# Performance work log

Hardware: AMD Instinct MI355X
Metric: run time of the kernel (lower is better)

The kernel has to match this reference:

```python
import jax, jax.numpy as jnp
import numpy as np

STATE_DIM = 512
N_AGENTS = 16
N_ACTIONS = 32
EMBED = 512          # mixing_embed_dim
Q_IN = STATE_DIM + N_AGENTS * N_ACTIONS  # 1024 (coma_critic arch)
ROWS = 32768         # bs * ts = 64 * 512


def _linear_params(key, d_in, d_out):
    kw, kb = jax.random.split(key)
    bound = 1.0 / np.sqrt(d_in)
    W = jax.random.uniform(kw, (d_in, d_out), minval=-bound, maxval=bound, dtype=jnp.float32)
    b = jax.random.uniform(kb, (d_out,), minval=-bound, maxval=bound, dtype=jnp.float32)
    return W, b


def setup_inputs() -> dict:
    key = jax.random.key(0)
    ks = jax.random.split(key, 8)
    states = jax.random.normal(ks[0], (ROWS, STATE_DIM), dtype=jnp.float32)
    actions = jax.random.uniform(ks[1], (ROWS, N_AGENTS * N_ACTIONS), dtype=jnp.float32)
    Qw1, Qb1 = _linear_params(ks[2], Q_IN, EMBED)
    Qw2, Qb2 = _linear_params(ks[3], EMBED, EMBED)
    Qw3, Qb3 = _linear_params(ks[4], EMBED, 1)
    Vw1, Vb1 = _linear_params(ks[5], STATE_DIM, EMBED)
    Vw2, Vb2 = _linear_params(ks[6], EMBED, EMBED)
    Vw3, Vb3 = _linear_params(ks[7], EMBED, 1)
    return {
        "states": states, "actions": actions,
        "Qw1": Qw1, "Qb1": Qb1, "Qw2": Qw2, "Qb2": Qb2, "Qw3": Qw3, "Qb3": Qb3,
        "Vw1": Vw1, "Vb1": Vb1, "Vw2": Vw2, "Vb2": Vb2, "Vw3": Vw3, "Vb3": Vb3,
    }


def _mlp3(x, W1, b1, W2, b2, W3, b3):
    h = jax.nn.relu(x @ W1 + b1)
    h = jax.nn.relu(h @ W2 + b2)
    return h @ W3 + b3


def reference(states, actions,
              Qw1, Qb1, Qw2, Qb2, Qw3, Qb3,
              Vw1, Vb1, Vw2, Vb2, Vw3, Vb3):
    # coma_critic arch: inputs = cat([states, joint-action one-hots], dim=1)
    inputs = jnp.concatenate([states, actions], axis=1)  # [bs*ts, Q_IN]
    q_outputs = _mlp3(inputs, Qw1, Qb1, Qw2, Qb2, Qw3, Qb3)  # [bs*ts, 1]
    v_outputs = _mlp3(states, Vw1, Vb1, Vw2, Vb2, Vw3, Vb3)  # [bs*ts, 1]
    return q_outputs, v_outputs
```

## Files before the change

### kernel.cpp

```cpp
#include <hip/hip_runtime.h>


#define ROWS 32768
#define EMBED 512

using frag_ab = __attribute__((ext_vector_type(8))) short;
using f32x4   = __attribute__((ext_vector_type(4))) float;

__device__ __forceinline__ unsigned short f2bf(float f) {
    unsigned int u = __builtin_bit_cast(unsigned int, f);
    return (unsigned short)((u + 0x7fffu + ((u >> 16) & 1u)) >> 16);
}

__device__ __forceinline__ unsigned pk2rne(float lo, float hi) {
    return (unsigned)f2bf(lo) | ((unsigned)f2bf(hi) << 16);
}

__device__ __forceinline__ void async_copy16(const void* g, void* l) {
    __builtin_amdgcn_global_load_lds(
        (const __attribute__((address_space(1))) unsigned int*)g,
        (__attribute__((address_space(3))) unsigned int*)l, 16, 0, 0);
}

__device__ __forceinline__ void decode_mn(int L, int& mi, int& nq) {
    nq = (L >> 3) & 7;
    mi = ((L >> 6) << 3) | (L & 7);
}

__global__ __launch_bounds__(256)
void prep(const float* __restrict__ states, const float* __restrict__ actions,
          const float* __restrict__ Qw1, const float* __restrict__ Qw2,
          const float* __restrict__ Vw1, const float* __restrict__ Vw2,
          const float* __restrict__ qb3, const float* __restrict__ vb3,
          unsigned short* __restrict__ X,
          unsigned short* __restrict__ Qw1t, unsigned short* __restrict__ Qw2t,
          unsigned short* __restrict__ Vw1t, unsigned short* __restrict__ Vw2t,
          float* __restrict__ out) {
    const int b = blockIdx.x, tid = threadIdx.x;
    if (b < 4096) {
        int c = b * 256 + tid;
        int m = c >> 5, col = (c & 31) * 32;
        const float* src = (col < 512) ? states + (size_t)m * 512 + col
                                       : actions + (size_t)m * 512 + (col - 512);
        float4 f[8];
#pragma unroll
        for (int i = 0; i < 8; i++) f[i] = ((const float4*)src)[i];
        uint4* dst = (uint4*)(X + (size_t)m * 1024 + col);
#pragma unroll
        for (int i = 0; i < 4; i++)
            dst[i] = make_uint4(pk2rne(f[2*i].x,   f[2*i].y),
                                pk2rne(f[2*i].z,   f[2*i].w),
                                pk2rne(f[2*i+1].x, f[2*i+1].y),
                                pk2rne(f[2*i+1].z, f[2*i+1].w));
    } else if (b < 4736) {
        int g = (b - 4096) * 256 + tid;
        const float* W; unsigned short* O; int n, k0, ldo;
        if (g < 65536) {
            int o = g * 8; n = o >> 10; k0 = o & 1023; W = Qw1; O = Qw1t; ldo = 1024;
        } else {
            g -= 65536;
            int seg = g >> 15, r = g & 32767, o = r * 8;
            n = o >> 9; k0 = o & 511; ldo = 512;
            W = (seg == 0) ? Qw2 : (seg == 1) ? Vw1 : Vw2;
            O = (seg == 0) ? Qw2t : (seg == 1) ? Vw1t : Vw2t;
        }
        float v[8];
#pragma unroll
        for (int j = 0; j < 8; j++) v[j] = W[(size_t)(k0 + j) * 512 + n];
        *(uint4*)(O + (size_t)n * ldo + k0) =
            make_uint4(pk2rne(v[0], v[1]), pk2rne(v[2], v[3]),
                       pk2rne(v[4], v[5]), pk2rne(v[6], v[7]));
    } else {
        int i = (b - 4736) * 256 + tid;
        out[i] = (i < ROWS) ? qb3[0] : vb3[0];
    }
}

__global__ __launch_bounds__(256)
void layer1(const unsigned short* __restrict__ X,
            const unsigned short* __restrict__ Qw1t,
            const unsigned short* __restrict__ Vw1t,
            const float* __restrict__ Qb1, const float* __restrict__ Vb1,
            unsigned short* __restrict__ h1Q, unsigned short* __restrict__ h1V) {
    __shared__ __align__(16) unsigned short As[2 * 4096];
    __shared__ __align__(16) unsigned short Bs[2 * 4096];

    const int tid = threadIdx.x, wave = tid >> 6, lane = tid & 63;
    int mi, nq; decode_mn(blockIdx.x, mi, nq);
    const bool isV = nq >= 4;
    const int bn = (nq & 3) * 128;
    const int bm = mi * 128;
    const int K = isV ? 512 : 1024;
    const unsigned short* Wt = isV ? Vw1t : Qw1t;
    const float* bias = isV ? Vb1 : Qb1;
    unsigned short* H = isV ? h1V : h1Q;

    const int wm = (wave & 1) * 64, wn = (wave >> 1) * 64;
    const int lrow = lane & 15, quad = lane >> 4;
    f32x4 acc[4][4] = {};

    const int lin  = wave * 1024 + lane * 16;
    const int rowS = lin >> 6, colS = (lin & 63) >> 1;
    const unsigned short* gA0 = X  + (size_t)(bm + rowS)      * 1024 + colS;
    const unsigned short* gA1 = X  + (size_t)(bm + rowS + 64) * 1024 + colS;
    const unsigned short* gB0 = Wt + (size_t)(bn + rowS)      * K + colS;
    const unsigned short* gB1 = Wt + (size_t)(bn + rowS + 64) * K + colS;
    unsigned short* ldsA0 = As + wave * 512;
    unsigned short* ldsA1 = As + 2048 + wave * 512;
    unsigned short* ldsB0 = Bs + wave * 512;
    unsigned short* ldsB1 = Bs + 2048 + wave * 512;

    for (int k0 = 0; k0 < K; k0 += 64) {
        async_copy16(gA0,      ldsA0);
        async_copy16(gA0 + 32, ldsA0 + 4096);
        async_copy16(gA1,      ldsA1);
        async_copy16(gA1 + 32, ldsA1 + 4096);
        async_copy16(gB0,      ldsB0);
        async_copy16(gB0 + 32, ldsB0 + 4096);
        async_copy16(gB1,      ldsB1);
        async_copy16(gB1 + 32, ldsB1 + 4096);
        gA0 += 64; gA1 += 64; gB0 += 64; gB1 += 64;
        __syncthreads();

#pragma unroll
        for (int s = 0; s < 2; s++) {
            frag_ab af[4], bfr[4];
#pragma unroll
            for (int i = 0; i < 4; i++)
                af[i] = *(const frag_ab*)&As[s * 4096 + (wm + i * 16 + lrow) * 32 + quad * 8];
#pragma unroll
            for (int j = 0; j < 4; j++)
                bfr[j] = *(const frag_ab*)&Bs[s * 4096 + (wn + j * 16 + lrow) * 32 + quad * 8];
#pragma unroll
            for (int i = 0; i < 4; i++)
#pragma unroll
                for (int j = 0; j < 4; j++)
                    acc[i][j] = __builtin_amdgcn_mfma_f32_16x16x32_bf16(
                        af[i], bfr[j], acc[i][j], 0, 0, 0);
        }
        __syncthreads();
    }

#pragma unroll
    for (int j = 0; j < 4; j++) {
        const int col = bn + wn + j * 16 + lrow;
        const float bc = bias[col];
#pragma unroll
        for (int i = 0; i < 4; i++) {
            const int row0 = bm + wm + i * 16 + quad * 4;
#pragma unroll
            for (int r = 0; r < 4; r++) {
                float v = acc[i][j][r] + bc;
                v = v > 0.0f ? v : 0.0f;
                H[(size_t)(row0 + r) * EMBED + col] = f2bf(v);
            }
        }
    }
}

__global__ __launch_bounds__(256)
void layer2(const unsigned short* __restrict__ h1Q,
            const unsigned short* __restrict__ h1V,
            const unsigned short* __restrict__ Qw2t,
            const unsigned short* __restrict__ Vw2t,
            const float* __restrict__ Qb2, const float* __restrict__ Vb2,
            const float* __restrict__ Qw3, const float* __restrict__ Vw3,
            float* __restrict__ out) {
    __shared__ __align__(16) unsigned short As[2 * 4096];
    __shared__ __align__(16) unsigned short Bs[2 * 4096];

    const int tid = threadIdx.x, wave = tid >> 6, lane = tid & 63;
    int mi, nq; decode_mn(blockIdx.x, mi, nq);
    const bool isV = nq >= 4;
    const int bn = (nq & 3) * 128;
    const int bm = mi * 128;
    const unsigned short* A  = isV ? h1V : h1Q;
    const unsigned short* Wt = isV ? Vw2t : Qw2t;
    const float* bias = isV ? Vb2 : Qb2;
    const float* w3   = isV ? Vw3 : Qw3;
    float* op = out + (isV ? ROWS : 0);

    const int wm = (wave & 1) * 64, wn = (wave >> 1) * 64;
    const int lrow = lane & 15, quad = lane >> 4;
    f32x4 acc[4][4] = {};

    const int lin  = wave * 1024 + lane * 16;
    const int rowS = lin >> 6, colS = (lin & 63) >> 1;
    const unsigned short* gA0 = A  + (size_t)(bm + rowS)      * 512 + colS;
    const unsigned short* gA1 = A  + (size_t)(bm + rowS + 64) * 512 + colS;
    const unsigned short* gB0 = Wt + (size_t)(bn + rowS)      * 512 + colS;
    const unsigned short* gB1 = Wt + (size_t)(bn + rowS + 64) * 512 + colS;
    unsigned short* ldsA0 = As + wave * 512;
    unsigned short* ldsA1 = As + 2048 + wave * 512;
    unsigned short* ldsB0 = Bs + wave * 512;
    unsigned short* ldsB1 = Bs + 2048 + wave * 512;

    for (int k0 = 0; k0 < 512; k0 += 64) {
        async_copy16(gA0,      ldsA0);
        async_copy16(gA0 + 32, ldsA0 + 4096);
        async_copy16(gA1,      ldsA1);
        async_copy16(gA1 + 32, ldsA1 + 4096);
        async_copy16(gB0,      ldsB0);
        async_copy16(gB0 + 32, ldsB0 + 4096);
        async_copy16(gB1,      ldsB1);
        async_copy16(gB1 + 32, ldsB1 + 4096);
        gA0 += 64; gA1 += 64; gB0 += 64; gB1 += 64;
        __syncthreads();

#pragma unroll
        for (int s = 0; s < 2; s++) {
            frag_ab af[4], bfr[4];
#pragma unroll
            for (int i = 0; i < 4; i++)
                af[i] = *(const frag_ab*)&As[s * 4096 + (wm + i * 16 + lrow) * 32 + quad * 8];
#pragma unroll
            for (int j = 0; j < 4; j++)
                bfr[j] = *(const frag_ab*)&Bs[s * 4096 + (wn + j * 16 + lrow) * 32 + quad * 8];
#pragma unroll
            for (int i = 0; i < 4; i++)
#pragma unroll
                for (int j = 0; j < 4; j++)
                    acc[i][j] = __builtin_amdgcn_mfma_f32_16x16x32_bf16(
                        af[i], bfr[j], acc[i][j], 0, 0, 0);
        }
        __syncthreads();
    }

    float bc[4], wc[4];
#pragma unroll
    for (int j = 0; j < 4; j++) {
        const int col = bn + wn + j * 16 + lrow;
        bc[j] = bias[col];
        wc[j] = w3[col];
    }
#pragma unroll
    for (int i = 0; i < 4; i++) {
#pragma unroll
        for (int r = 0; r < 4; r++) {
            float s = 0.0f;
#pragma unroll
            for (int j = 0; j < 4; j++) {
                float v = acc[i][j][r] + bc[j];
                v = v > 0.0f ? v : 0.0f;
                s += v * wc[j];
            }
#pragma unroll
            for (int m = 1; m < 16; m <<= 1) s += __shfl_xor(s, m, 64);
            if (lrow == 0)
                atomicAdd(&op[bm + wm + i * 16 + quad * 4 + r], s);
        }
    }
}

extern "C" void kernel_launch(void* const* d_in, const int* in_sizes, int n_in,
                              void* d_out, int out_size, void* d_ws, size_t ws_size,
                              hipStream_t stream) {
    const float* states  = (const float*)d_in[0];
    const float* actions = (const float*)d_in[1];
    const float* Qw1 = (const float*)d_in[2];
    const float* Qb1 = (const float*)d_in[3];
    const float* Qw2 = (const float*)d_in[4];
    const float* Qb2 = (const float*)d_in[5];
    const float* Qw3 = (const float*)d_in[6];
    const float* Qb3 = (const float*)d_in[7];
    const float* Vw1 = (const float*)d_in[8];
    const float* Vb1 = (const float*)d_in[9];
    const float* Vw2 = (const float*)d_in[10];
    const float* Vb2 = (const float*)d_in[11];
    const float* Vw3 = (const float*)d_in[12];
    const float* Vb3 = (const float*)d_in[13];
    float* out = (float*)d_out;

    char* ws = (char*)d_ws;
    unsigned short* X    = (unsigned short*)ws;
    unsigned short* h1Q  = (unsigned short*)(ws + 67108864);
    unsigned short* h1V  = (unsigned short*)(ws + 100663296);
    unsigned short* Qw1t = (unsigned short*)(ws + 134217728);
    unsigned short* Qw2t = Qw1t + 512 * 1024;
    unsigned short* Vw1t = Qw2t + 512 * 512;
    unsigned short* Vw2t = Vw1t + 512 * 512;

    prep<<<dim3(4992), dim3(256), 0, stream>>>(states, actions, Qw1, Qw2, Vw1, Vw2,
                                               Qb3, Vb3, X, Qw1t, Qw2t, Vw1t, Vw2t, out);

    layer1<<<dim3(2048), dim3(256), 0, stream>>>(X, Qw1t, Vw1t, Qb1, Vb1, h1Q, h1V);
    layer2<<<dim3(2048), dim3(256), 0, stream>>>(h1Q, h1V, Qw2t, Vw2t, Qb2, Vb2, Qw3, Vw3, out);
}
```

Measured before the change: 304.3 us.

## Fuse fp32-to-bf16 input conversion into layer1 and drop LDS staging in GEMMs

Removes the separate pass that converted states and actions into a bf16 concatenated buffer. Layer1 now reads fp32 activations straight from global memory and packs them into MFMA fragments in registers. Both GEMM kernels drop the LDS async-copy staging and its barriers, loading fragments directly from global memory, and gain a min-blocks launch bound. The weight transpose is rewritten as an LDS-tiled transpose. The trade-off is no data sharing through LDS, so each wave re-reads A and B tiles through cache with narrower, strided loads.

```diff
diff --git a/kernel.cpp b/kernel.cpp
--- a/kernel.cpp
+++ b/kernel.cpp
@@ -16,10 +16,11 @@
     return (unsigned)f2bf(lo) | ((unsigned)f2bf(hi) << 16);
 }
 
-__device__ __forceinline__ void async_copy16(const void* g, void* l) {
-    __builtin_amdgcn_global_load_lds(
-        (const __attribute__((address_space(1))) unsigned int*)g,
-        (__attribute__((address_space(3))) unsigned int*)l, 16, 0, 0);
+__device__ __forceinline__ frag_ab pack8(float4 a, float4 b) {
+    union { frag_ab f; unsigned u[4]; } r;
+    r.u[0] = pk2rne(a.x, a.y); r.u[1] = pk2rne(a.z, a.w);
+    r.u[2] = pk2rne(b.x, b.y); r.u[3] = pk2rne(b.z, b.w);
+    return r.f;
 }
 
 __device__ __forceinline__ void decode_mn(int L, int& mi, int& nq) {
@@ -28,69 +29,52 @@
 }
 
 __global__ __launch_bounds__(256)
-void prep(const float* __restrict__ states, const float* __restrict__ actions,
-          const float* __restrict__ Qw1, const float* __restrict__ Qw2,
+void prep(const float* __restrict__ Qw1, const float* __restrict__ Qw2,
           const float* __restrict__ Vw1, const float* __restrict__ Vw2,
           const float* __restrict__ qb3, const float* __restrict__ vb3,
-          unsigned short* __restrict__ X,
           unsigned short* __restrict__ Qw1t, unsigned short* __restrict__ Qw2t,
           unsigned short* __restrict__ Vw1t, unsigned short* __restrict__ Vw2t,
           float* __restrict__ out) {
     const int b = blockIdx.x, tid = threadIdx.x;
-    if (b < 4096) {
-        int c = b * 256 + tid;
-        int m = c >> 5, col = (c & 31) * 32;
-        const float* src = (col < 512) ? states + (size_t)m * 512 + col
-                                       : actions + (size_t)m * 512 + (col - 512);
-        float4 f[8];
-#pragma unroll
-        for (int i = 0; i < 8; i++) f[i] = ((const float4*)src)[i];
-        uint4* dst = (uint4*)(X + (size_t)m * 1024 + col);
-#pragma unroll
-        for (int i = 0; i < 4; i++)
-            dst[i] = make_uint4(pk2rne(f[2*i].x,   f[2*i].y),
-                                pk2rne(f[2*i].z,   f[2*i].w),
-                                pk2rne(f[2*i+1].x, f[2*i+1].y),
-                                pk2rne(f[2*i+1].z, f[2*i+1].w));
-    } else if (b < 4736) {
-        int g = (b - 4096) * 256 + tid;
-        const float* W; unsigned short* O; int n, k0, ldo;
-        if (g < 65536) {
-            int o = g * 8; n = o >> 10; k0 = o & 1023; W = Qw1; O = Qw1t; ldo = 1024;
-        } else {
-            g -= 65536;
-            int seg = g >> 15, r = g & 32767, o = r * 8;
-            n = o >> 9; k0 = o & 511; ldo = 512;
-            W = (seg == 0) ? Qw2 : (seg == 1) ? Vw1 : Vw2;
-            O = (seg == 0) ? Qw2t : (seg == 1) ? Vw1t : Vw2t;
-        }
-        float v[8];
-#pragma unroll
-        for (int j = 0; j < 8; j++) v[j] = W[(size_t)(k0 + j) * 512 + n];
-        *(uint4*)(O + (size_t)n * ldo + k0) =
-            make_uint4(pk2rne(v[0], v[1]), pk2rne(v[2], v[3]),
-                       pk2rne(v[4], v[5]), pk2rne(v[6], v[7]));
+    if (b < 320) {
+        __shared__ unsigned short T[64 * 65];
+        const float* W; unsigned short* O; int ldo, kt, nt;
+        if (b < 128) { W = Qw1; O = Qw1t; ldo = 1024; kt = b >> 3; nt = b & 7; }
+        else {
+            int c = b - 128, which = c >> 6, r = c & 63;
+            kt = r >> 3; nt = r & 7; ldo = 512;
+            W = (which == 0) ? Qw2 : (which == 1) ? Vw1 : Vw2;
+            O = (which == 0) ? Qw2t : (which == 1) ? Vw1t : Vw2t;
+        }
+        const int k0 = kt * 64, n0 = nt * 64;
+#pragma unroll
+        for (int p = 0; p < 16; p++) {
+            int e = tid + p * 256, kr = e >> 6, nc = e & 63;
+            T[nc * 65 + kr] = f2bf(W[(size_t)(k0 + kr) * 512 + n0 + nc]);
+        }
+        __syncthreads();
+#pragma unroll
+        for (int p = 0; p < 16; p++) {
+            int e = tid + p * 256, nr = e >> 6, kc = e & 63;
+            O[(size_t)(n0 + nr) * ldo + k0 + kc] = T[nr * 65 + kc];
+        }
     } else {
-        int i = (b - 4736) * 256 + tid;
+        int i = (b - 320) * 256 + tid;
         out[i] = (i < ROWS) ? qb3[0] : vb3[0];
     }
 }
 
-__global__ __launch_bounds__(256)
-void layer1(const unsigned short* __restrict__ X,
+__global__ __launch_bounds__(256, 3)
+void layer1(const float* __restrict__ states, const float* __restrict__ actions,
             const unsigned short* __restrict__ Qw1t,
             const unsigned short* __restrict__ Vw1t,
             const float* __restrict__ Qb1, const float* __restrict__ Vb1,
             unsigned short* __restrict__ h1Q, unsigned short* __restrict__ h1V) {
-    __shared__ __align__(16) unsigned short As[2 * 4096];
-    __shared__ __align__(16) unsigned short Bs[2 * 4096];
-
     const int tid = threadIdx.x, wave = tid >> 6, lane = tid & 63;
     int mi, nq; decode_mn(blockIdx.x, mi, nq);
     const bool isV = nq >= 4;
-    const int bn = (nq & 3) * 128;
-    const int bm = mi * 128;
-    const int K = isV ? 512 : 1024;
+    const int bn = (nq & 3) * 128, bm = mi * 128;
+    const int ldb = isV ? 512 : 1024;
     const unsigned short* Wt = isV ? Vw1t : Qw1t;
     const float* bias = isV ? Vb1 : Qb1;
     unsigned short* H = isV ? h1V : h1Q;
@@ -99,46 +83,57 @@
     const int lrow = lane & 15, quad = lane >> 4;
     f32x4 acc[4][4] = {};
 
-    const int lin  = wave * 1024 + lane * 16;
-    const int rowS = lin >> 6, colS = (lin & 63) >> 1;
-    const unsigned short* gA0 = X  + (size_t)(bm + rowS)      * 1024 + colS;
-    const unsigned short* gA1 = X  + (size_t)(bm + rowS + 64) * 1024 + colS;
-    const unsigned short* gB0 = Wt + (size_t)(bn + rowS)      * K + colS;
-    const unsigned short* gB1 = Wt + (size_t)(bn + rowS + 64) * K + colS;
-    unsigned short* ldsA0 = As + wave * 512;
-    unsigned short* ldsA1 = As + 2048 + wave * 512;
-    unsigned short* ldsB0 = Bs + wave * 512;
-    unsigned short* ldsB1 = Bs + 2048 + wave * 512;
-
-    for (int k0 = 0; k0 < K; k0 += 64) {
-        async_copy16(gA0,      ldsA0);
-        async_copy16(gA0 + 32, ldsA0 + 4096);
-        async_copy16(gA1,      ldsA1);
-        async_copy16(gA1 + 32, ldsA1 + 4096);
-        async_copy16(gB0,      ldsB0);
-        async_copy16(gB0 + 32, ldsB0 + 4096);
-        async_copy16(gB1,      ldsB1);
-        async_copy16(gB1 + 32, ldsB1 + 4096);
-        gA0 += 64; gA1 += 64; gB0 += 64; gB1 += 64;
-        __syncthreads();
-
-#pragma unroll
-        for (int s = 0; s < 2; s++) {
-            frag_ab af[4], bfr[4];
-#pragma unroll
-            for (int i = 0; i < 4; i++)
-                af[i] = *(const frag_ab*)&As[s * 4096 + (wm + i * 16 + lrow) * 32 + quad * 8];
+    const float* aRow[4];
+    const unsigned short* bRow[4];
+#pragma unroll
+    for (int i = 0; i < 4; i++)
+        aRow[i] = states + (size_t)(bm + wm + i * 16 + lrow) * 512 + quad * 8;
+#pragma unroll
+    for (int j = 0; j < 4; j++)
+        bRow[j] = Wt + (size_t)(bn + wn + j * 16 + lrow) * ldb + quad * 8;
+
+#pragma unroll 2
+    for (int k = 0; k < 512; k += 32) {
+        frag_ab af[4], bf[4];
+#pragma unroll
+        for (int i = 0; i < 4; i++) {
+            float4 x = *(const float4*)(aRow[i] + k);
+            float4 y = *(const float4*)(aRow[i] + k + 4);
+            af[i] = pack8(x, y);
+        }
+#pragma unroll
+        for (int j = 0; j < 4; j++) bf[j] = *(const frag_ab*)(bRow[j] + k);
+#pragma unroll
+        for (int i = 0; i < 4; i++)
 #pragma unroll
             for (int j = 0; j < 4; j++)
-                bfr[j] = *(const frag_ab*)&Bs[s * 4096 + (wn + j * 16 + lrow) * 32 + quad * 8];
+                acc[i][j] = __builtin_amdgcn_mfma_f32_16x16x32_bf16(
+                    af[i], bf[j], acc[i][j], 0, 0, 0);
+    }
+
+    if (!isV) {
+        const float* a2[4];
+#pragma unroll
+        for (int i = 0; i < 4; i++)
+            a2[i] = actions + (size_t)(bm + wm + i * 16 + lrow) * 512 + quad * 8;
+#pragma unroll 2
+        for (int k = 0; k < 512; k += 32) {
+            frag_ab af[4], bf[4];
+#pragma unroll
+            for (int i = 0; i < 4; i++) {
+                float4 x = *(const float4*)(a2[i] + k);
+                float4 y = *(const float4*)(a2[i] + k + 4);
+                af[i] = pack8(x, y);
+            }
+#pragma unroll
+            for (int j = 0; j < 4; j++) bf[j] = *(const frag_ab*)(bRow[j] + 512 + k);
 #pragma unroll
             for (int i = 0; i < 4; i++)
 #pragma unroll
                 for (int j = 0; j < 4; j++)
                     acc[i][j] = __builtin_amdgcn_mfma_f32_16x16x32_bf16(
-                        af[i], bfr[j], acc[i][j], 0, 0, 0);
-        }
-        __syncthreads();
+                        af[i], bf[j], acc[i][j], 0, 0, 0);
+        }
     }
 
 #pragma unroll
@@ -158,7 +153,7 @@
     }
 }
 
-__global__ __launch_bounds__(256)
+__global__ __launch_bounds__(256, 3)
 void layer2(const unsigned short* __restrict__ h1Q,
             const unsigned short* __restrict__ h1V,
             const unsigned short* __restrict__ Qw2t,
@@ -166,14 +161,10 @@
             const float* __restrict__ Qb2, const float* __restrict__ Vb2,
             const float* __restrict__ Qw3, const float* __restrict__ Vw3,
             float* __restrict__ out) {
-    __shared__ __align__(16) unsigned short As[2 * 4096];
-    __shared__ __align__(16) unsigned short Bs[2 * 4096];
-
     const int tid = threadIdx.x, wave = tid >> 6, lane = tid & 63;
     int mi, nq; decode_mn(blockIdx.x, mi, nq);
     const bool isV = nq >= 4;
-    const int bn = (nq & 3) * 128;
-    const int bm = mi * 128;
+    const int bn = (nq & 3) * 128, bm = mi * 128;
     const unsigned short* A  = isV ? h1V : h1Q;
     const unsigned short* Wt = isV ? Vw2t : Qw2t;
     const float* bias = isV ? Vb2 : Qb2;
@@ -184,46 +175,28 @@
     const int lrow = lane & 15, quad = lane >> 4;
     f32x4 acc[4][4] = {};
 
-    const int lin  = wave * 1024 + lane * 16;
-    const int rowS = lin >> 6, colS = (lin & 63) >> 1;
-    const unsigned short* gA0 = A  + (size_t)(bm + rowS)      * 512 + colS;
-    const unsigned short* gA1 = A  + (size_t)(bm + rowS + 64) * 512 + colS;
-    const unsigned short* gB0 = Wt + (size_t)(bn + rowS)      * 512 + colS;
-    const unsigned short* gB1 = Wt + (size_t)(bn + rowS + 64) * 512 + colS;
-    unsigned short* ldsA0 = As + wave * 512;
-    unsigned short* ldsA1 = As + 2048 + wave * 512;
-    unsigned short* ldsB0 = Bs + wave * 512;
-    unsigned short* ldsB1 = Bs + 2048 + wave * 512;
-
-    for (int k0 = 0; k0 < 512; k0 += 64) {
-        async_copy16(gA0,      ldsA0);
-        async_copy16(gA0 + 32, ldsA0 + 4096);
-        async_copy16(gA1,      ldsA1);
-        async_copy16(gA1 + 32, ldsA1 + 4096);
-        async_copy16(gB0,      ldsB0);
-        async_copy16(gB0 + 32, ldsB0 + 4096);
-        async_copy16(gB1,      ldsB1);
-        async_copy16(gB1 + 32, ldsB1 + 4096);
-        gA0 += 64; gA1 += 64; gB0 += 64; gB1 += 64;
-        __syncthreads();
-
-#pragma unroll
-        for (int s = 0; s < 2; s++) {
-            frag_ab af[4], bfr[4];
-#pragma unroll
-            for (int i = 0; i < 4; i++)
-                af[i] = *(const frag_ab*)&As[s * 4096 + (wm + i * 16 + lrow) * 32 + quad * 8];
+    const unsigned short* aRow[4];
+    const unsigned short* bRow[4];
+#pragma unroll
+    for (int i = 0; i < 4; i++)
+        aRow[i] = A + (size_t)(bm + wm + i * 16 + lrow) * 512 + quad * 8;
+#pragma unroll
+    for (int j = 0; j < 4; j++)
+        bRow[j] = Wt + (size_t)(bn + wn + j * 16 + lrow) * 512 + quad * 8;
+
+#pragma unroll 2
+    for (int k = 0; k < 512; k += 32) {
+        frag_ab af[4], bf[4];
+#pragma unroll
+        for (int i = 0; i < 4; i++) af[i] = *(const frag_ab*)(aRow[i] + k);
+#pragma unroll
+        for (int j = 0; j < 4; j++) bf[j] = *(const frag_ab*)(bRow[j] + k);
+#pragma unroll
+        for (int i = 0; i < 4; i++)
 #pragma unroll
             for (int j = 0; j < 4; j++)
-                bfr[j] = *(const frag_ab*)&Bs[s * 4096 + (wn + j * 16 + lrow) * 32 + quad * 8];
-#pragma unroll
-            for (int i = 0; i < 4; i++)
-#pragma unroll
-                for (int j = 0; j < 4; j++)
-                    acc[i][j] = __builtin_amdgcn_mfma_f32_16x16x32_bf16(
-                        af[i], bfr[j], acc[i][j], 0, 0, 0);
-        }
-        __syncthreads();
+                acc[i][j] = __builtin_amdgcn_mfma_f32_16x16x32_bf16(
+                    af[i], bf[j], acc[i][j], 0, 0, 0);
     }
 
     float bc[4], wc[4];
@@ -272,17 +245,18 @@
     float* out = (float*)d_out;
 
     char* ws = (char*)d_ws;
-    unsigned short* X    = (unsigned short*)ws;
-    unsigned short* h1Q  = (unsigned short*)(ws + 67108864);
-    unsigned short* h1V  = (unsigned short*)(ws + 100663296);
-    unsigned short* Qw1t = (unsigned short*)(ws + 134217728);
+    unsigned short* h1Q  = (unsigned short*)ws;
+    unsigned short* h1V  = (unsigned short*)(ws + 33554432);
+    unsigned short* Qw1t = (unsigned short*)(ws + 67108864);
     unsigned short* Qw2t = Qw1t + 512 * 1024;
     unsigned short* Vw1t = Qw2t + 512 * 512;
     unsigned short* Vw2t = Vw1t + 512 * 512;
 
-    prep<<<dim3(4992), dim3(256), 0, stream>>>(states, actions, Qw1, Qw2, Vw1, Vw2,
-                                               Qb3, Vb3, X, Qw1t, Qw2t, Vw1t, Vw2t, out);
-
-    layer1<<<dim3(2048), dim3(256), 0, stream>>>(X, Qw1t, Vw1t, Qb1, Vb1, h1Q, h1V);
-    layer2<<<dim3(2048), dim3(256), 0, stream>>>(h1Q, h1V, Qw2t, Vw2t, Qb2, Vb2, Qw3, Vw3, out);
-}
+    prep<<<dim3(576), dim3(256), 0, stream>>>(Qw1, Qw2, Vw1, Vw2, Qb3, Vb3,
+                                              Qw1t, Qw2t, Vw1t, Vw2t, out);
+
+    layer1<<<dim3(2048), dim3(256), 0, stream>>>(states, actions, Qw1t, Vw1t,
+                                                 Qb1, Vb1, h1Q, h1V);
+    layer2<<<dim3(2048), dim3(256), 0, stream>>>(h1Q, h1V, Qw2t, Vw2t,
+                                                 Qb2, Vb2, Qw3, Vw3, out);
+}
```

Measured after the change: 579.7 us. 1.9x slower.
